# Kernel tuning notes

Hardware: AMD Instinct MI355X
Metric: run time of the kernel (lower is better)

The kernel has to match this reference:

```python
import jax, jax.numpy as jnp
import numpy as np

B, T, D, H = 2048, 200, 64, 64


def setup_inputs() -> dict:
    key = jax.random.key(0)
    ks = jax.random.split(key, 5)
    rnn_input = jax.random.normal(ks[0], (B, T, D), dtype=jnp.float32)
    sequence_length = jax.random.randint(ks[1], (B,), 0, T, dtype=jnp.int32)
    att_score = jax.random.uniform(ks[2], (B, T, 1), dtype=jnp.float32)
    # glorot-uniform-style init for kernels; TF VecAttGRUCell uses constant 1.0 gate bias
    s = np.float32(np.sqrt(6.0 / (D + H + 2 * H)))
    gate_kernel = jax.random.uniform(ks[3], (D + H, 2 * H), jnp.float32, -s, s)
    gate_bias = jnp.ones((2 * H,), jnp.float32)
    sc = np.float32(np.sqrt(6.0 / (D + H + H)))
    cand_kernel = jax.random.uniform(ks[4], (D + H, H), jnp.float32, -sc, sc)
    cand_bias = jnp.zeros((H,), jnp.float32)
    return dict(rnn_input=rnn_input, sequence_length=sequence_length,
                att_score=att_score, gate_kernel=gate_kernel, gate_bias=gate_bias,
                cand_kernel=cand_kernel, cand_bias=cand_bias)


def _augru(rnn_input, sequence_length, att_score, gate_kernel, gate_bias, cand_kernel, cand_bias):
    # rnn_input: [B,T,D], att_score: [B,T,1], sequence_length: [B]
    Bn, Tn, _ = rnn_input.shape
    Hn = cand_kernel.shape[1]
    x_t = jnp.swapaxes(rnn_input, 0, 1)   # [T,B,D]
    a_t = jnp.swapaxes(att_score, 0, 1)   # [T,B,1]
    t_idx = jnp.arange(Tn)
    h0 = jnp.zeros((Bn, Hn), rnn_input.dtype)

    def step(h, inp):
        x, a, t = inp
        gates = jax.nn.sigmoid(jnp.concatenate([x, h], axis=-1) @ gate_kernel + gate_bias)
        r, u = jnp.split(gates, 2, axis=-1)                       # [B,H] each
        c = jnp.tanh(jnp.concatenate([x, r * h], axis=-1) @ cand_kernel + cand_bias)
        u_hat = (1.0 - a) * u                                      # attention-modulated update gate
        new_h = u_hat * h + (1.0 - u_hat) * c
        valid = (t < sequence_length)[:, None]                     # dynamic_rnn semantics
        h_next = jnp.where(valid, new_h, h)                        # freeze state past seq len
        out = jnp.where(valid, new_h, jnp.zeros_like(new_h))       # zero outputs past seq len
        return h_next, out

    h_last, outs = jax.lax.scan(step, h0, (x_t, a_t, t_idx))
    return jnp.swapaxes(outs, 0, 1), h_last  # [B,T,H], [B,H]


def reference(rnn_input, sequence_length, att_score, gate_kernel, gate_bias, cand_kernel, cand_bias):
    outputs, _ = _augru(rnn_input, sequence_length, att_score,
                        gate_kernel, gate_bias, cand_kernel, cand_bias)
    return outputs  # return_sequence=True
```

## Files before the change

kernel.cpp:

```cpp
#include <hip/hip_runtime.h>

#define Tn 200
#define Dn 64
#define Hn 64
#define CC 16

typedef _Float16 half2v __attribute__((ext_vector_type(2)));
typedef _Float16 half8v __attribute__((ext_vector_type(8)));
typedef float    f32x4  __attribute__((ext_vector_type(4)));
typedef unsigned int uint;

__device__ __forceinline__ float fast_sigmoid(float v) {
    return __builtin_amdgcn_rcpf(1.0f + __expf(-v));
}
__device__ __forceinline__ float fast_tanh(float v) {
    return 1.0f - 2.0f * __builtin_amdgcn_rcpf(1.0f + __expf(2.0f * v));
}
__device__ __forceinline__ void cfence() {
    asm volatile("" ::: "memory");
}
__device__ __forceinline__ void wave_lds_fence() {
    asm volatile("s_waitcnt lgkmcnt(0)" ::: "memory");
}

__device__ __forceinline__ half8v cvt8(const float4 a, const float4 b) {
    return half8v{(_Float16)a.x, (_Float16)a.y, (_Float16)a.z, (_Float16)a.w,
                  (_Float16)b.x, (_Float16)b.y, (_Float16)b.z, (_Float16)b.w};
}

__global__ __launch_bounds__(64, 1)
void augru_proj_mfma(const float* __restrict__ x,
                     const int*   __restrict__ slen,
                     const float* __restrict__ gk,
                     const float* __restrict__ gb,
                     const float* __restrict__ ck,
                     const float* __restrict__ cb,
                     _Float16*    __restrict__ P,
                     int nsub)
{
    const int lane = threadIdx.x;
    const int lm   = lane & 15;
    const int kq   = lane >> 4;

    __shared__ __align__(16) _Float16 sbuf[16][200];

    half8v bf[12][2];
    float  bias[12];
#pragma unroll
    for (int nt = 0; nt < 12; ++nt) {
        const int n = nt * 16 + lm;
#pragma unroll
        for (int kh = 0; kh < 2; ++kh) {
            half8v f;
#pragma unroll
            for (int e = 0; e < 8; ++e) {
                const int k = kh * 32 + kq * 8 + e;
                f[e] = (_Float16)((n < 128) ? gk[k * 128 + n]
                                            : ck[k * 64 + (n - 128)]);
            }
            bf[nt][kh] = f;
        }
        bias[nt] = (n < 128) ? gb[n] : cb[n - 128];
    }

    for (int s = blockIdx.x; s < nsub; s += gridDim.x) {
        const int rb = s * 16;

        const int rowv = rb + lm;
        const int bv   = rowv / Tn;
        const int tv   = rowv - bv * Tn;
        if (__ballot(tv < slen[bv]) == 0ull) continue;

        const float* xr = x + (size_t)rowv * Dn + kq * 8;
        const float4 q0 = *(const float4*)(xr);
        const float4 q1 = *(const float4*)(xr + 4);
        const float4 q2 = *(const float4*)(xr + 32);
        const float4 q3 = *(const float4*)(xr + 36);
        const half8v a0 = cvt8(q0, q1);
        const half8v a1 = cvt8(q2, q3);

#pragma unroll
        for (int nt = 0; nt < 12; ++nt) {
            f32x4 c = {bias[nt], bias[nt], bias[nt], bias[nt]};
            c = __builtin_amdgcn_mfma_f32_16x16x32_f16(a0, bf[nt][0], c, 0, 0, 0);
            c = __builtin_amdgcn_mfma_f32_16x16x32_f16(a1, bf[nt][1], c, 0, 0, 0);
#pragma unroll
            for (int r = 0; r < 4; ++r)
                sbuf[kq * 4 + r][nt * 16 + lm] = (_Float16)c[r];
        }
        cfence();

#pragma unroll
        for (int i = 0; i < 6; ++i) {
            const int idx = i * 64 + lane;
            const int row = idx / 24;
            const int c16 = idx % 24;
            const uint4 v = *(const uint4*)&sbuf[row][c16 * 8];
            *(uint4*)(P + (size_t)(rb + row) * 192 + c16 * 8) = v;
        }
        cfence();
    }
}

__global__ __launch_bounds__(64, 2)
void augru_rec(const _Float16* __restrict__ P,
               const int*     __restrict__ slen,
               const float*   __restrict__ att,
               const float*   __restrict__ gk,
               const float*   __restrict__ ck,
               float*         __restrict__ out)
{
    const int b = blockIdx.x;
    const int j = threadIdx.x;

    __shared__ __align__(16) _Float16 s_h[Hn];
    __shared__ __align__(16) _Float16 s_rh[Hn];

    half2v wr[32], wu[32], wc[32];
#pragma unroll
    for (int m = 0; m < 32; ++m) {
        const int k = 64 + 2 * m;
        wr[m] = half2v{(_Float16)gk[(k + 0) * 128 + j],
                       (_Float16)gk[(k + 1) * 128 + j]};
        wu[m] = half2v{(_Float16)gk[(k + 0) * 128 + 64 + j],
                       (_Float16)gk[(k + 1) * 128 + 64 + j]};
        wc[m] = half2v{(_Float16)ck[(k + 0) * 64 + j],
                       (_Float16)ck[(k + 1) * 64 + j]};
    }

    const int len = slen[b];
    const _Float16* Prow = P   + (size_t)b * Tn * 192;
    const float*    arow = att + (size_t)b * Tn;
    float*          orow = out + (size_t)b * Tn * Hn;

    float h = 0.0f;

    _Float16 pr_n = (_Float16)0, pu_n = (_Float16)0, pc_n = (_Float16)0;
    float a_n = 0.0f;
    if (len > 0) {
        pr_n = Prow[j]; pu_n = Prow[64 + j]; pc_n = Prow[128 + j];
        a_n  = arow[0];
    }

    for (int t = 0; t < len; ++t) {
        const float pr = (float)pr_n;
        const float pu = (float)pu_n;
        const float pc = (float)pc_n;
        const float a  = a_n;
        const int tn = min(t + 1, len - 1);
        const _Float16* Pt = Prow + (size_t)tn * 192;
        pr_n = Pt[j]; pu_n = Pt[64 + j]; pc_n = Pt[128 + j];
        a_n  = arow[tn];

        s_h[j] = (_Float16)h;
        cfence();

        float r0 = pr, r1 = 0.f, u0 = pu, u1 = 0.f;
        const half8v* hv = (const half8v*)s_h;
#pragma unroll
        for (int m8 = 0; m8 < 8; ++m8) {
            const half8v v = hv[m8];
            const half2v p0 = __builtin_shufflevector(v, v, 0, 1);
            const half2v p1 = __builtin_shufflevector(v, v, 2, 3);
            const half2v p2 = __builtin_shufflevector(v, v, 4, 5);
            const half2v p3 = __builtin_shufflevector(v, v, 6, 7);
            const int m = m8 * 4;
            r0 = __builtin_amdgcn_fdot2(p0, wr[m + 0], r0, false);
            r1 = __builtin_amdgcn_fdot2(p1, wr[m + 1], r1, false);
            r0 = __builtin_amdgcn_fdot2(p2, wr[m + 2], r0, false);
            r1 = __builtin_amdgcn_fdot2(p3, wr[m + 3], r1, false);
            u0 = __builtin_amdgcn_fdot2(p0, wu[m + 0], u0, false);
            u1 = __builtin_amdgcn_fdot2(p1, wu[m + 1], u1, false);
            u0 = __builtin_amdgcn_fdot2(p2, wu[m + 2], u0, false);
            u1 = __builtin_amdgcn_fdot2(p3, wu[m + 3], u1, false);
        }
        const float rg = fast_sigmoid(r0 + r1);
        const float ug = fast_sigmoid(u0 + u1);

        s_rh[j] = (_Float16)(rg * h);
        cfence();

        float c0 = pc, c1 = 0.f;
        const half8v* rv = (const half8v*)s_rh;
#pragma unroll
        for (int m8 = 0; m8 < 8; ++m8) {
            const half8v v = rv[m8];
            const half2v p0 = __builtin_shufflevector(v, v, 0, 1);
            const half2v p1 = __builtin_shufflevector(v, v, 2, 3);
            const half2v p2 = __builtin_shufflevector(v, v, 4, 5);
            const half2v p3 = __builtin_shufflevector(v, v, 6, 7);
            const int m = m8 * 4;
            c0 = __builtin_amdgcn_fdot2(p0, wc[m + 0], c0, false);
            c1 = __builtin_amdgcn_fdot2(p1, wc[m + 1], c1, false);
            c0 = __builtin_amdgcn_fdot2(p2, wc[m + 2], c0, false);
            c1 = __builtin_amdgcn_fdot2(p3, wc[m + 3], c1, false);
        }
        const float cg = fast_tanh(c0 + c1);

        const float uh = (1.0f - a) * ug;
        h = uh * h + (1.0f - uh) * cg;
        orow[t * Hn + j] = h;
        cfence();
    }

    float4 z;
    z.x = z.y = z.z = z.w = 0.0f;
    float* tail = orow + (size_t)len * Hn;
    const int total = (Tn - len) * Hn;
    for (int i = j * 4; i < total; i += 64 * 4) {
        *(float4*)(tail + i) = z;
    }
}

__global__ __launch_bounds__(128, 2)
void augru_fused_fb(const float* __restrict__ x, const int* __restrict__ slen,
                    const float* __restrict__ att, const float* __restrict__ gk,
                    const float* __restrict__ gb, const float* __restrict__ ck,
                    const float* __restrict__ cb, float* __restrict__ out)
{
    const int b    = blockIdx.x;
    const int tid  = threadIdx.x;
    const int wave = tid >> 6;
    const int j    = tid & 63;

    __shared__ float s_P[2][CC][3][Hn];
    __shared__ __align__(16) _Float16 s_h[Hn];
    __shared__ __align__(16) _Float16 s_rh[Hn];

    const int len     = slen[b];
    const int nchunks = (len + CC - 1) / CC;
    const float* xrow = x   + (size_t)b * Tn * Dn;
    const float* arow = att + (size_t)b * Tn;
    float*       orow = out + (size_t)b * Tn * Hn;

    if (wave == 0) {
        half2v wr[32], wu[32], wc[32];
#pragma unroll
        for (int m = 0; m < 32; ++m) {
            const int k = 2 * m;
            wr[m] = half2v{(_Float16)gk[(k + 0) * 128 + j], (_Float16)gk[(k + 1) * 128 + j]};
            wu[m] = half2v{(_Float16)gk[(k + 0) * 128 + 64 + j], (_Float16)gk[(k + 1) * 128 + 64 + j]};
            wc[m] = half2v{(_Float16)ck[(k + 0) * 64 + j], (_Float16)ck[(k + 1) * 64 + j]};
        }
        const float br = gb[j], bu = gb[64 + j], bc = cb[j];
        for (int c = 0; c < nchunks; ++c) {
            const int t0 = c * CC, tend = min(len, t0 + CC);
            for (int t = t0; t < tend; ++t) {
                const float4* xv = (const float4*)(xrow + t * Dn);
                float r0 = br, r1 = 0.f, u0 = bu, u1 = 0.f, c0 = bc, c1 = 0.f;
#pragma unroll
                for (int kk = 0; kk < 16; ++kk) {
                    const float4 q = xv[kk];
                    const half2v p0 = half2v{(_Float16)q.x, (_Float16)q.y};
                    const half2v p1 = half2v{(_Float16)q.z, (_Float16)q.w};
                    const int m = 2 * kk;
                    r0 = __builtin_amdgcn_fdot2(p0, wr[m], r0, false);
                    r1 = __builtin_amdgcn_fdot2(p1, wr[m + 1], r1, false);
                    u0 = __builtin_amdgcn_fdot2(p0, wu[m], u0, false);
                    u1 = __builtin_amdgcn_fdot2(p1, wu[m + 1], u1, false);
                    c0 = __builtin_amdgcn_fdot2(p0, wc[m], c0, false);
                    c1 = __builtin_amdgcn_fdot2(p1, wc[m + 1], c1, false);
                }
                const int lt = t - t0;
                s_P[c & 1][lt][0][j] = r0 + r1;
                s_P[c & 1][lt][1][j] = u0 + u1;
                s_P[c & 1][lt][2][j] = c0 + c1;
            }
            __syncthreads();
        }
    } else {
        half2v wr[32], wu[32], wc[32];
#pragma unroll
        for (int m = 0; m < 32; ++m) {
            const int k = 64 + 2 * m;
            wr[m] = half2v{(_Float16)gk[(k + 0) * 128 + j], (_Float16)gk[(k + 1) * 128 + j]};
            wu[m] = half2v{(_Float16)gk[(k + 0) * 128 + 64 + j], (_Float16)gk[(k + 1) * 128 + 64 + j]};
            wc[m] = half2v{(_Float16)ck[(k + 0) * 64 + j], (_Float16)ck[(k + 1) * 64 + j]};
        }
        float h = 0.0f;
        for (int c = 0; c < nchunks; ++c) {
            __syncthreads();
            const int t0 = c * CC, tend = min(len, t0 + CC);
            for (int t = t0; t < tend; ++t) {
                const int lt = t - t0;
                const float pr = s_P[c & 1][lt][0][j];
                const float pu = s_P[c & 1][lt][1][j];
                const float pc = s_P[c & 1][lt][2][j];
                const float a  = arow[t];
                s_h[j] = (_Float16)h;
                wave_lds_fence();
                float r0 = pr, r1 = 0.f, u0 = pu, u1 = 0.f;
                const half8v* hv = (const half8v*)s_h;
#pragma unroll
                for (int m8 = 0; m8 < 8; ++m8) {
                    const half8v v = hv[m8];
                    const half2v p0 = __builtin_shufflevector(v, v, 0, 1);
                    const half2v p1 = __builtin_shufflevector(v, v, 2, 3);
                    const half2v p2 = __builtin_shufflevector(v, v, 4, 5);
                    const half2v p3 = __builtin_shufflevector(v, v, 6, 7);
                    const int m = m8 * 4;
                    r0 = __builtin_amdgcn_fdot2(p0, wr[m + 0], r0, false);
                    r1 = __builtin_amdgcn_fdot2(p1, wr[m + 1], r1, false);
                    r0 = __builtin_amdgcn_fdot2(p2, wr[m + 2], r0, false);
                    r1 = __builtin_amdgcn_fdot2(p3, wr[m + 3], r1, false);
                    u0 = __builtin_amdgcn_fdot2(p0, wu[m + 0], u0, false);
                    u1 = __builtin_amdgcn_fdot2(p1, wu[m + 1], u1, false);
                    u0 = __builtin_amdgcn_fdot2(p2, wu[m + 2], u0, false);
                    u1 = __builtin_amdgcn_fdot2(p3, wu[m + 3], u1, false);
                }
                const float rg = fast_sigmoid(r0 + r1);
                const float ug = fast_sigmoid(u0 + u1);
                s_rh[j] = (_Float16)(rg * h);
                wave_lds_fence();
                float c0 = pc, c1 = 0.f;
                const half8v* rv = (const half8v*)s_rh;
#pragma unroll
                for (int m8 = 0; m8 < 8; ++m8) {
                    const half8v v = rv[m8];
                    const half2v p0 = __builtin_shufflevector(v, v, 0, 1);
                    const half2v p1 = __builtin_shufflevector(v, v, 2, 3);
                    const half2v p2 = __builtin_shufflevector(v, v, 4, 5);
                    const half2v p3 = __builtin_shufflevector(v, v, 6, 7);
                    const int m = m8 * 4;
                    c0 = __builtin_amdgcn_fdot2(p0, wc[m + 0], c0, false);
                    c1 = __builtin_amdgcn_fdot2(p1, wc[m + 1], c1, false);
                    c0 = __builtin_amdgcn_fdot2(p2, wc[m + 2], c0, false);
                    c1 = __builtin_amdgcn_fdot2(p3, wc[m + 3], c1, false);
                }
                const float cg = fast_tanh(c0 + c1);
                const float uh = (1.0f - a) * ug;
                h = uh * h + (1.0f - uh) * cg;
                orow[t * Hn + j] = h;
                wave_lds_fence();
            }
        }
    }
    float4 z; z.x = z.y = z.z = z.w = 0.0f;
    float* tail = orow + len * Hn;
    const int total = (Tn - len) * Hn;
    for (int i = tid * 4; i < total; i += 128 * 4) *(float4*)(tail + i) = z;
}

extern "C" void kernel_launch(void* const* d_in, const int* in_sizes, int n_in,
                              void* d_out, int out_size, void* d_ws, size_t ws_size,
                              hipStream_t stream) {
    const float* x    = (const float*)d_in[0];
    const int*   slen = (const int*)  d_in[1];
    const float* att  = (const float*)d_in[2];
    const float* gk   = (const float*)d_in[3];
    const float* gb   = (const float*)d_in[4];
    const float* ck   = (const float*)d_in[5];
    const float* cb   = (const float*)d_in[6];
    float* out = (float*)d_out;

    const int B = in_sizes[1];
    const size_t needP = (size_t)B * Tn * 192 * sizeof(_Float16);

    if (ws_size >= needP) {
        _Float16* P = (_Float16*)d_ws;
        const int nrows = B * Tn;
        const int nsub  = nrows / 16;
        const int grid  = nsub < 8192 ? nsub : 8192;
        augru_proj_mfma<<<grid, 64, 0, stream>>>(x, slen, gk, gb, ck, cb, P, nsub);
        augru_rec<<<B, 64, 0, stream>>>(P, slen, att, gk, ck, out);
    } else {
        augru_fused_fb<<<B, 128, 0, stream>>>(x, slen, att, gk, gb, ck, cb, out);
    }
}
```

Before: 350.6 us.

## Prefetch next x tile in projection kernel and reorder recurrent dot products

```diff
diff --git a/kernel.cpp b/kernel.cpp
--- a/kernel.cpp
+++ b/kernel.cpp
@@ -41,6 +41,7 @@
     const int lane = threadIdx.x;
     const int lm   = lane & 15;
     const int kq   = lane >> 4;
+    const int G    = gridDim.x;
 
     __shared__ __align__(16) _Float16 sbuf[16][200];
 
@@ -63,42 +64,57 @@
         bias[nt] = (n < 128) ? gb[n] : cb[n - 128];
     }
 
-    for (int s = blockIdx.x; s < nsub; s += gridDim.x) {
-        const int rb = s * 16;
-
+    float4 qa0{}, qa1{}, qa2{}, qa3{};
+    if (blockIdx.x < nsub) {
+        const float* xr = x + (size_t)(blockIdx.x * 16 + lm) * Dn + kq * 8;
+        qa0 = *(const float4*)(xr);
+        qa1 = *(const float4*)(xr + 4);
+        qa2 = *(const float4*)(xr + 32);
+        qa3 = *(const float4*)(xr + 36);
+    }
+
+    for (int s = blockIdx.x; s < nsub; s += G) {
+        float4 qb0{}, qb1{}, qb2{}, qb3{};
+        const int sn = s + G;
+        if (sn < nsub) {
+            const float* xr = x + (size_t)(sn * 16 + lm) * Dn + kq * 8;
+            qb0 = *(const float4*)(xr);
+            qb1 = *(const float4*)(xr + 4);
+            qb2 = *(const float4*)(xr + 32);
+            qb3 = *(const float4*)(xr + 36);
+        }
+
+        const int rb   = s * 16;
         const int rowv = rb + lm;
         const int bv   = rowv / Tn;
         const int tv   = rowv - bv * Tn;
-        if (__ballot(tv < slen[bv]) == 0ull) continue;
-
-        const float* xr = x + (size_t)rowv * Dn + kq * 8;
-        const float4 q0 = *(const float4*)(xr);
-        const float4 q1 = *(const float4*)(xr + 4);
-        const float4 q2 = *(const float4*)(xr + 32);
-        const float4 q3 = *(const float4*)(xr + 36);
-        const half8v a0 = cvt8(q0, q1);
-        const half8v a1 = cvt8(q2, q3);
-
-#pragma unroll
-        for (int nt = 0; nt < 12; ++nt) {
-            f32x4 c = {bias[nt], bias[nt], bias[nt], bias[nt]};
-            c = __builtin_amdgcn_mfma_f32_16x16x32_f16(a0, bf[nt][0], c, 0, 0, 0);
-            c = __builtin_amdgcn_mfma_f32_16x16x32_f16(a1, bf[nt][1], c, 0, 0, 0);
-#pragma unroll
-            for (int r = 0; r < 4; ++r)
-                sbuf[kq * 4 + r][nt * 16 + lm] = (_Float16)c[r];
-        }
-        cfence();
-
-#pragma unroll
-        for (int i = 0; i < 6; ++i) {
-            const int idx = i * 64 + lane;
-            const int row = idx / 24;
-            const int c16 = idx % 24;
-            const uint4 v = *(const uint4*)&sbuf[row][c16 * 8];
-            *(uint4*)(P + (size_t)(rb + row) * 192 + c16 * 8) = v;
-        }
-        cfence();
+        if (__ballot(tv < slen[bv]) != 0ull) {
+            const half8v a0 = cvt8(qa0, qa1);
+            const half8v a1 = cvt8(qa2, qa3);
+
+#pragma unroll
+            for (int nt = 0; nt < 12; ++nt) {
+                f32x4 c = {bias[nt], bias[nt], bias[nt], bias[nt]};
+                c = __builtin_amdgcn_mfma_f32_16x16x32_f16(a0, bf[nt][0], c, 0, 0, 0);
+                c = __builtin_amdgcn_mfma_f32_16x16x32_f16(a1, bf[nt][1], c, 0, 0, 0);
+#pragma unroll
+                for (int r = 0; r < 4; ++r)
+                    sbuf[kq * 4 + r][nt * 16 + lm] = (_Float16)c[r];
+            }
+            cfence();
+
+#pragma unroll
+            for (int i = 0; i < 6; ++i) {
+                const int idx = i * 64 + lane;
+                const int row = idx / 24;
+                const int c16 = idx % 24;
+                const uint4 v = *(const uint4*)&sbuf[row][c16 * 8];
+                *(uint4*)(P + (size_t)(rb + row) * 192 + c16 * 8) = v;
+            }
+            cfence();
+        }
+
+        qa0 = qb0; qa1 = qb1; qa2 = qb2; qa3 = qb3;
     }
 }
 
@@ -155,32 +171,45 @@
         s_h[j] = (_Float16)h;
         cfence();
 
-        float r0 = pr, r1 = 0.f, u0 = pu, u1 = 0.f;
         const half8v* hv = (const half8v*)s_h;
-#pragma unroll
-        for (int m8 = 0; m8 < 8; ++m8) {
-            const half8v v = hv[m8];
-            const half2v p0 = __builtin_shufflevector(v, v, 0, 1);
-            const half2v p1 = __builtin_shufflevector(v, v, 2, 3);
-            const half2v p2 = __builtin_shufflevector(v, v, 4, 5);
-            const half2v p3 = __builtin_shufflevector(v, v, 6, 7);
-            const int m = m8 * 4;
-            r0 = __builtin_amdgcn_fdot2(p0, wr[m + 0], r0, false);
-            r1 = __builtin_amdgcn_fdot2(p1, wr[m + 1], r1, false);
-            r0 = __builtin_amdgcn_fdot2(p2, wr[m + 2], r0, false);
-            r1 = __builtin_amdgcn_fdot2(p3, wr[m + 3], r1, false);
-            u0 = __builtin_amdgcn_fdot2(p0, wu[m + 0], u0, false);
-            u1 = __builtin_amdgcn_fdot2(p1, wu[m + 1], u1, false);
-            u0 = __builtin_amdgcn_fdot2(p2, wu[m + 2], u0, false);
-            u1 = __builtin_amdgcn_fdot2(p3, wu[m + 3], u1, false);
-        }
-        const float rg = fast_sigmoid(r0 + r1);
-        const float ug = fast_sigmoid(u0 + u1);
+        const half8v v0 = hv[0], v1 = hv[1], v2 = hv[2], v3 = hv[3];
+        const half8v v4 = hv[4], v5 = hv[5], v6 = hv[6], v7 = hv[7];
+
+        float r0 = pr, r1 = 0.f, r2 = 0.f, r3 = 0.f;
+#define RDOT(v, m)                                                        \
+        {   const half2v p0 = __builtin_shufflevector(v, v, 0, 1);        \
+            const half2v p1 = __builtin_shufflevector(v, v, 2, 3);        \
+            const half2v p2 = __builtin_shufflevector(v, v, 4, 5);        \
+            const half2v p3 = __builtin_shufflevector(v, v, 6, 7);        \
+            r0 = __builtin_amdgcn_fdot2(p0, wr[m + 0], r0, false);        \
+            r1 = __builtin_amdgcn_fdot2(p1, wr[m + 1], r1, false);        \
+            r2 = __builtin_amdgcn_fdot2(p2, wr[m + 2], r2, false);        \
+            r3 = __builtin_amdgcn_fdot2(p3, wr[m + 3], r3, false);        }
+        RDOT(v0, 0)  RDOT(v1, 4)  RDOT(v2, 8)  RDOT(v3, 12)
+        RDOT(v4, 16) RDOT(v5, 20) RDOT(v6, 24) RDOT(v7, 28)
+#undef RDOT
+        const float rg = fast_sigmoid((r0 + r1) + (r2 + r3));
 
         s_rh[j] = (_Float16)(rg * h);
         cfence();
 
-        float c0 = pc, c1 = 0.f;
+        float u0 = pu, u1 = 0.f, u2 = 0.f, u3 = 0.f;
+#define UDOT(v, m)                                                        \
+        {   const half2v p0 = __builtin_shufflevector(v, v, 0, 1);        \
+            const half2v p1 = __builtin_shufflevector(v, v, 2, 3);        \
+            const half2v p2 = __builtin_shufflevector(v, v, 4, 5);        \
+            const half2v p3 = __builtin_shufflevector(v, v, 6, 7);        \
+            u0 = __builtin_amdgcn_fdot2(p0, wu[m + 0], u0, false);        \
+            u1 = __builtin_amdgcn_fdot2(p1, wu[m + 1], u1, false);        \
+            u2 = __builtin_amdgcn_fdot2(p2, wu[m + 2], u2, false);        \
+            u3 = __builtin_amdgcn_fdot2(p3, wu[m + 3], u3, false);        }
+        UDOT(v0, 0)  UDOT(v1, 4)  UDOT(v2, 8)  UDOT(v3, 12)
+        UDOT(v4, 16) UDOT(v5, 20) UDOT(v6, 24) UDOT(v7, 28)
+#undef UDOT
+        const float ug = fast_sigmoid((u0 + u1) + (u2 + u3));
+        const float uh = (1.0f - a) * ug;
+
+        float c0 = pc, c1 = 0.f, c2 = 0.f, c3 = 0.f;
         const half8v* rv = (const half8v*)s_rh;
 #pragma unroll
         for (int m8 = 0; m8 < 8; ++m8) {
@@ -192,12 +221,11 @@
             const int m = m8 * 4;
             c0 = __builtin_amdgcn_fdot2(p0, wc[m + 0], c0, false);
             c1 = __builtin_amdgcn_fdot2(p1, wc[m + 1], c1, false);
-            c0 = __builtin_amdgcn_fdot2(p2, wc[m + 2], c0, false);
-            c1 = __builtin_amdgcn_fdot2(p3, wc[m + 3], c1, false);
-        }
-        const float cg = fast_tanh(c0 + c1);
-
-        const float uh = (1.0f - a) * ug;
+            c2 = __builtin_amdgcn_fdot2(p2, wc[m + 2], c2, false);
+            c3 = __builtin_amdgcn_fdot2(p3, wc[m + 3], c3, false);
+        }
+        const float cg = fast_tanh((c0 + c1) + (c2 + c3));
+
         h = uh * h + (1.0f - uh) * cg;
         orow[t * Hn + j] = h;
         cfence();
@@ -360,8 +388,7 @@
         _Float16* P = (_Float16*)d_ws;
         const int nrows = B * Tn;
         const int nsub  = nrows / 16;
-        const int grid  = nsub < 8192 ? nsub : 8192;
-        augru_proj_mfma<<<grid, 64, 0, stream>>>(x, slen, gk, gb, ck, cb, P, nsub);
+        augru_proj_mfma<<<2048, 64, 0, stream>>>(x, slen, gk, gb, ck, cb, P, nsub);
         augru_rec<<<B, 64, 0, stream>>>(P, slen, att, gk, ck, out);
     } else {
         augru_fused_fb<<<B, 128, 0, stream>>>(x, slen, att, gk, gb, ck, cb, out);
```

After: 374.3 us. 1.07x slower.
